# Optimization experiments

Measured on AMD Instinct MI355X. Metric: run time of the kernel, lower is better.

Reference implementation:

```python
import jax, jax.numpy as jnp
import numpy as np

B, M, D = 16384, 32, 16
LAYERS = [64, 64, 64]


def setup_inputs() -> dict:
    key = jax.random.key(0)
    ks = jax.random.split(key, 4)
    inp = {"embeddings": jax.random.normal(ks[0], (B, M, D), dtype=jnp.float32)}
    hk_1 = M
    for i, hk in enumerate(LAYERS):
        # glorot-ish scale for W_i of shape (m, Hk_1, Hk)
        scale = (2.0 / (M * hk_1 + hk)) ** 0.5
        inp[f"W{i}"] = jax.random.normal(ks[i + 1], (M, hk_1, hk), dtype=jnp.float32) * scale
        hk_1 = hk
    return inp


def reference(embeddings, W0, W1, W2):
    # embeddings == x0: (B, m, D); W_i: (m, Hk_1, Hk)
    x0 = embeddings
    xk = x0  # x^{k-1}, starts as x0 with Hk_1 = m
    outs = []
    for W in (W0, W1, W2):
        # Fused form of: (x0[:,:,None,:] * xk[:,None,:,:])[..., None] * W -> sum over m, Hk_1
        # then permute to (B, Hk, D) and apply activation.
        xk = jax.nn.relu(jnp.einsum("bmd,bhd,mhk->bkd", x0, xk, W))  # (B, Hk, D)
        outs.append(jnp.sum(xk, axis=2))  # (B, Hk)
    return jnp.concatenate(outs, axis=1)  # (B, sum(layers_dim))
```

## Files before the change

kernel.cpp:

```cpp
#include <hip/hip_runtime.h>


typedef _Float16 half8 __attribute__((ext_vector_type(8)));
typedef _Float16 half2v __attribute__((ext_vector_type(2)));
typedef float f32x4 __attribute__((ext_vector_type(4)));

#define OUT_STRIDE 192
#define X0R 33
#define X0B (16 * X0R)
#define XKR 72
#define XKB 1152

__global__ void prep_w_all(const float* __restrict__ W0,
                           const float* __restrict__ W1,
                           const float* __restrict__ W2,
                           _Float16* __restrict__ dst) {
  __shared__ float tile[32 * 65];
  const int tid = threadIdx.x;
  const int blk = blockIdx.x;
  const float* src;
  _Float16* d;
  int kb;
  if (blk < 32)      { src = W0 + (size_t)blk * 2048;        d = dst;          kb = blk; }
  else if (blk < 96) { src = W1 + (size_t)(blk - 32) * 2048; d = dst + 65536;  kb = blk - 32; }
  else               { src = W2 + (size_t)(blk - 96) * 2048; d = dst + 196608; kb = blk - 96; }
#pragma unroll
  for (int i = tid; i < 2048; i += 256)
    tile[(i >> 6) * 65 + (i & 63)] = src[i];
  __syncthreads();
  const int lane = tid & 63, t = tid >> 6;
  const int qq = lane >> 4, n = t * 16 + (lane & 15);
  half8 v;
#pragma unroll
  for (int j = 0; j < 8; ++j)
    v[j] = (_Float16)tile[(qq * 8 + j) * 65 + n];
  *(half8*)(d + (size_t)kb * 2048 + tid * 8) = v;
}

template<int NHI, bool LAST>
__device__ __forceinline__ void run_layer(
    const _Float16* __restrict__ Wp, const half8 (&av)[4][NHI],
    const _Float16* x0row0, _Float16* xkw, float* __restrict__ out,
    long gb0, int loff, int lane, int r, int q)
{
  f32x4 acc[4][4];
#pragma unroll
  for (int b = 0; b < 4; ++b)
#pragma unroll
    for (int t = 0; t < 4; ++t) acc[b][t] = (f32x4){0.f, 0.f, 0.f, 0.f};

#pragma unroll 2
  for (int m = 0; m < 32; ++m) {
    half2v xs2[4];
#pragma unroll
    for (int b = 0; b < 4; ++b) {
      _Float16 x = x0row0[b * X0B + m];
      xs2[b] = (half2v){x, x};
    }
#pragma unroll
    for (int hi = 0; hi < NHI; ++hi) {
      const int kb = m * NHI + hi;
      const _Float16* pkb = Wp + (size_t)kb * 2048 + lane * 8;
      half8 Bf[4];
#pragma unroll
      for (int t = 0; t < 4; ++t)
        Bf[t] = *(const half8*)(pkb + t * 512);
#pragma unroll
      for (int b = 0; b < 4; ++b) {
        half8 af;
        half2v* ap = (half2v*)&af;
        const half2v* vp = (const half2v*)&av[b][hi];
#pragma unroll
        for (int j2 = 0; j2 < 4; ++j2) ap[j2] = vp[j2] * xs2[b];
#pragma unroll
        for (int t = 0; t < 4; ++t)
          acc[b][t] = __builtin_amdgcn_mfma_f32_16x16x32_f16(
              af, Bf[t], acc[b][t], 0, 0, 0);
      }
    }
  }

#pragma unroll
  for (int b = 0; b < 4; ++b) {
#pragma unroll
    for (int t = 0; t < 4; ++t) {
      float s = 0.f;
#pragma unroll
      for (int rr = 0; rr < 4; ++rr) {
        float v = acc[b][t][rr];
        v = v > 0.f ? v : 0.f;
        s += v;
        if (!LAST)
          xkw[b * XKB + (q * 4 + rr) * XKR + t * 16 + r] = (_Float16)v;
      }
      s += __shfl_xor(s, 16);
      s += __shfl_xor(s, 32);
      if (q == 0)
        out[(gb0 + b) * OUT_STRIDE + loff + t * 16 + r] = s;
    }
  }
}

__global__ __launch_bounds__(256, 3) void cin_main(
    const float* __restrict__ emb, const _Float16* __restrict__ Wall,
    float* __restrict__ out)
{
  __shared__ __align__(16) _Float16 lds[16 * X0B + 16 * XKB];
  const int lane = threadIdx.x & 63;
  const int wv = threadIdx.x >> 6;
  const int r = lane & 15, q = lane >> 4;
  const long gb0 = (long)blockIdx.x * 16 + wv * 4;

  _Float16* x0w = &lds[wv * 4 * X0B];
  _Float16* xkw = &lds[16 * X0B + wv * 4 * XKB];

#pragma unroll
  for (int bb = 0; bb < 4; ++bb) {
    const float* src = emb + (gb0 + bb) * 512;
    _Float16* dstb = x0w + bb * X0B;
#pragma unroll
    for (int i = 0; i < 2; ++i) {
      int f = i * 256 + lane * 4;
      float4 v = *(const float4*)(src + f);
      int m = f >> 4, d = f & 15;
      dstb[(d + 0) * X0R + m] = (_Float16)v.x;
      dstb[(d + 1) * X0R + m] = (_Float16)v.y;
      dstb[(d + 2) * X0R + m] = (_Float16)v.z;
      dstb[(d + 3) * X0R + m] = (_Float16)v.w;
    }
  }

  const _Float16* x0row0 = x0w + r * X0R;

  half8 av1[4][1];
#pragma unroll
  for (int b = 0; b < 4; ++b)
#pragma unroll
    for (int j = 0; j < 8; ++j)
      av1[b][0][j] = x0row0[b * X0B + q * 8 + j];
  run_layer<1, false>(Wall, av1, x0row0, xkw, out, gb0, 0, lane, r, q);

  half8 av2[4][2];
#pragma unroll
  for (int b = 0; b < 4; ++b)
#pragma unroll
    for (int hi = 0; hi < 2; ++hi)
      av2[b][hi] = *(const half8*)(xkw + b * XKB + r * XKR + hi * 32 + q * 8);
  run_layer<2, false>(Wall + 65536, av2, x0row0, xkw, out, gb0, 64, lane, r, q);

#pragma unroll
  for (int b = 0; b < 4; ++b)
#pragma unroll
    for (int hi = 0; hi < 2; ++hi)
      av2[b][hi] = *(const half8*)(xkw + b * XKB + r * XKR + hi * 32 + q * 8);
  run_layer<2, true>(Wall + 196608, av2, x0row0, xkw, out, gb0, 128, lane, r, q);
}

extern "C" void kernel_launch(void* const* d_in, const int* in_sizes, int n_in,
                              void* d_out, int out_size, void* d_ws, size_t ws_size,
                              hipStream_t stream) {
  const float* emb = (const float*)d_in[0];
  const float* W0  = (const float*)d_in[1];
  const float* W1  = (const float*)d_in[2];
  const float* W2  = (const float*)d_in[3];
  float* out = (float*)d_out;
  _Float16* ws = (_Float16*)d_ws;

  prep_w_all<<<160, 256, 0, stream>>>(W0, W1, W2, ws);

  cin_main<<<1024, 256, 0, stream>>>(emb, ws, out);
}
```

Measured before the change: 209.9 us.

## Double-buffer W fragment loads and stagger m start per wave

Restructures the m-loop into a register double-buffered pipeline that prefetches the next m's weight fragments and x0 scalars while issuing MFMAs on the current ones. Each wave starts at a rotated m offset so waves spread their global weight reads across different addresses. It also uses an inline v_pk_mul_f16 with op_sel to broadcast the x0 scalar, and lowers launch bounds from 3 to 2 waves per SIMD so the extra registers fit. Lower occupancy may expose latency that the prefetching does not cover.

```diff
diff --git a/kernel.cpp b/kernel.cpp
--- a/kernel.cpp
+++ b/kernel.cpp
@@ -10,6 +10,13 @@
 #define X0B (16 * X0R)
 #define XKR 72
 #define XKB 1152
+
+__device__ __forceinline__ half2v pk_mul_bcast(half2v a, unsigned int xs) {
+  half2v r;
+  asm("v_pk_mul_f16 %0, %1, %2 op_sel:[0,0] op_sel_hi:[1,0]"
+      : "=v"(r) : "v"(a), "v"(xs));
+  return r;
+}
 
 __global__ void prep_w_all(const float* __restrict__ W0,
                            const float* __restrict__ W1,
@@ -41,7 +48,7 @@
 __device__ __forceinline__ void run_layer(
     const _Float16* __restrict__ Wp, const half8 (&av)[4][NHI],
     const _Float16* x0row0, _Float16* xkw, float* __restrict__ out,
-    long gb0, int loff, int lane, int r, int q)
+    long gb0, int loff, int lane, int r, int q, int mstart)
 {
   f32x4 acc[4][4];
 #pragma unroll
@@ -49,36 +56,67 @@
 #pragma unroll
     for (int t = 0; t < 4; ++t) acc[b][t] = (f32x4){0.f, 0.f, 0.f, 0.f};
 
-#pragma unroll 2
-  for (int m = 0; m < 32; ++m) {
-    half2v xs2[4];
-#pragma unroll
-    for (int b = 0; b < 4; ++b) {
-      _Float16 x = x0row0[b * X0B + m];
-      xs2[b] = (half2v){x, x};
+  const _Float16* Wl = Wp + lane * 8;
+
+#define LOADB(DST, MM)                                                      \
+  {                                                                         \
+    const _Float16* p_ = Wl + (size_t)(MM) * (NHI * 2048);                  \
+    _Pragma("unroll")                                                       \
+    for (int hi = 0; hi < NHI; ++hi)                                        \
+      _Pragma("unroll")                                                     \
+      for (int t = 0; t < 4; ++t)                                           \
+        DST[hi][t] = *(const half8*)(p_ + hi * 2048 + t * 512);             \
+  }
+
+#define LOADXS(DST, MM)                                                     \
+  {                                                                         \
+    _Pragma("unroll")                                                       \
+    for (int b = 0; b < 4; ++b)                                             \
+      DST[b] = *(const unsigned short*)(x0row0 + b * X0B + (MM));           \
+  }
+
+#define COMPUTE(BB, XX)                                                     \
+  {                                                                         \
+    _Pragma("unroll")                                                       \
+    for (int b = 0; b < 4; ++b) {                                           \
+      _Pragma("unroll")                                                     \
+      for (int hi = 0; hi < NHI; ++hi) {                                    \
+        half8 af;                                                           \
+        half2v* ap = (half2v*)&af;                                          \
+        const half2v* vp = (const half2v*)&av[b][hi];                       \
+        _Pragma("unroll")                                                   \
+        for (int j2 = 0; j2 < 4; ++j2)                                      \
+          ap[j2] = pk_mul_bcast(vp[j2], XX[b]);                             \
+        _Pragma("unroll")                                                   \
+        for (int t = 0; t < 4; ++t)                                         \
+          acc[b][t] = __builtin_amdgcn_mfma_f32_16x16x32_f16(               \
+              af, BB[hi][t], acc[b][t], 0, 0, 0);                           \
+      }                                                                     \
+    }                                                                       \
+  }
+
+  half8 Bc[NHI][4], Bn[NHI][4];
+  unsigned int xc[4], xn[4];
+  const int m0 = mstart;
+
+  LOADB(Bc, m0);
+  LOADXS(xc, m0);
+
+  for (int s = 0; s < 32; s += 2) {
+    const int m1 = (m0 + s + 1) & 31;
+    LOADB(Bn, m1);
+    LOADXS(xn, m1);
+    COMPUTE(Bc, xc);
+    if (s < 30) {
+      const int m2 = (m0 + s + 2) & 31;
+      LOADB(Bc, m2);
+      LOADXS(xc, m2);
     }
-#pragma unroll
-    for (int hi = 0; hi < NHI; ++hi) {
-      const int kb = m * NHI + hi;
-      const _Float16* pkb = Wp + (size_t)kb * 2048 + lane * 8;
-      half8 Bf[4];
-#pragma unroll
-      for (int t = 0; t < 4; ++t)
-        Bf[t] = *(const half8*)(pkb + t * 512);
-#pragma unroll
-      for (int b = 0; b < 4; ++b) {
-        half8 af;
-        half2v* ap = (half2v*)&af;
-        const half2v* vp = (const half2v*)&av[b][hi];
-#pragma unroll
-        for (int j2 = 0; j2 < 4; ++j2) ap[j2] = vp[j2] * xs2[b];
-#pragma unroll
-        for (int t = 0; t < 4; ++t)
-          acc[b][t] = __builtin_amdgcn_mfma_f32_16x16x32_f16(
-              af, Bf[t], acc[b][t], 0, 0, 0);
-      }
-    }
-  }
+    COMPUTE(Bn, xn);
+  }
+#undef LOADB
+#undef LOADXS
+#undef COMPUTE
 
 #pragma unroll
   for (int b = 0; b < 4; ++b) {
@@ -101,7 +139,7 @@
   }
 }
 
-__global__ __launch_bounds__(256, 3) void cin_main(
+__global__ __launch_bounds__(256, 2) void cin_main(
     const float* __restrict__ emb, const _Float16* __restrict__ Wall,
     float* __restrict__ out)
 {
@@ -110,6 +148,8 @@
   const int wv = threadIdx.x >> 6;
   const int r = lane & 15, q = lane >> 4;
   const long gb0 = (long)blockIdx.x * 16 + wv * 4;
+
+  const int mstart = ((blockIdx.x + wv) & 3) * 8;
 
   _Float16* x0w = &lds[wv * 4 * X0B];
   _Float16* xkw = &lds[16 * X0B + wv * 4 * XKB];
@@ -138,7 +178,7 @@
 #pragma unroll
     for (int j = 0; j < 8; ++j)
       av1[b][0][j] = x0row0[b * X0B + q * 8 + j];
-  run_layer<1, false>(Wall, av1, x0row0, xkw, out, gb0, 0, lane, r, q);
+  run_layer<1, false>(Wall, av1, x0row0, xkw, out, gb0, 0, lane, r, q, mstart);
 
   half8 av2[4][2];
 #pragma unroll
@@ -146,14 +186,14 @@
 #pragma unroll
     for (int hi = 0; hi < 2; ++hi)
       av2[b][hi] = *(const half8*)(xkw + b * XKB + r * XKR + hi * 32 + q * 8);
-  run_layer<2, false>(Wall + 65536, av2, x0row0, xkw, out, gb0, 64, lane, r, q);
+  run_layer<2, false>(Wall + 65536, av2, x0row0, xkw, out, gb0, 64, lane, r, q, mstart);
 
 #pragma unroll
   for (int b = 0; b < 4; ++b)
 #pragma unroll
     for (int hi = 0; hi < 2; ++hi)
       av2[b][hi] = *(const half8*)(xkw + b * XKB + r * XKR + hi * 32 + q * 8);
-  run_layer<2, true>(Wall + 196608, av2, x0row0, xkw, out, gb0, 128, lane, r, q);
+  run_layer<2, true>(Wall + 196608, av2, x0row0, xkw, out, gb0, 128, lane, r, q, mstart);
 }
 
 extern "C" void kernel_launch(void* const* d_in, const int* in_sizes, int n_in,
```

New measurement: 224.0 us. 6.7% more time.

## Switch CIN matmuls from 16x16x32 to 32x32x16 MFMA with paired batch rows

Applied to the files above, without the earlier changes.

Replaces the 16x16x32 f16 MFMA tiling with 32x32x16 MFMA. Each A tile now packs two batch elements' 16 D-rows into 32 rows, and the weight prep kernel is re-laid-out to match the 32-wide B fragments. This halves the number of weight fragment loads per MFMA and the MFMA instruction count, aiming for higher matrix-core efficiency. The epilogue remapping and the XK LDS stride change (72 to 64, removing padding) risk more LDS bank conflicts, and the new index mapping adds risk to correctness.

```diff
diff --git a/kernel.cpp b/kernel.cpp
--- a/kernel.cpp
+++ b/kernel.cpp
@@ -3,13 +3,13 @@
 
 typedef _Float16 half8 __attribute__((ext_vector_type(8)));
 typedef _Float16 half2v __attribute__((ext_vector_type(2)));
-typedef float f32x4 __attribute__((ext_vector_type(4)));
+typedef float f32x16 __attribute__((ext_vector_type(16)));
 
 #define OUT_STRIDE 192
 #define X0R 33
 #define X0B (16 * X0R)
-#define XKR 72
-#define XKB 1152
+#define XKR 64
+#define XKB 1024
 
 __global__ void prep_w_all(const float* __restrict__ W0,
                            const float* __restrict__ W1,
@@ -20,83 +20,92 @@
   const int blk = blockIdx.x;
   const float* src;
   _Float16* d;
-  int kb;
-  if (blk < 32)      { src = W0 + (size_t)blk * 2048;        d = dst;          kb = blk; }
-  else if (blk < 96) { src = W1 + (size_t)(blk - 32) * 2048; d = dst + 65536;  kb = blk - 32; }
-  else               { src = W2 + (size_t)(blk - 96) * 2048; d = dst + 196608; kb = blk - 96; }
+  int bl;
+  if (blk < 32)      { src = W0; d = dst;          bl = blk; }
+  else if (blk < 96) { src = W1; d = dst + 65536;  bl = blk - 32; }
+  else               { src = W2; d = dst + 196608; bl = blk - 96; }
+  src += (size_t)bl * 2048;
+  d   += (size_t)bl * 2048;
 #pragma unroll
   for (int i = tid; i < 2048; i += 256)
     tile[(i >> 6) * 65 + (i & 63)] = src[i];
   __syncthreads();
-  const int lane = tid & 63, t = tid >> 6;
-  const int qq = lane >> 4, n = t * 16 + (lane & 15);
+  const int sub  = tid >> 7;
+  const int t    = (tid >> 6) & 1;
+  const int lane = tid & 63;
+  const int q2 = lane >> 5, l31 = lane & 31;
   half8 v;
 #pragma unroll
   for (int j = 0; j < 8; ++j)
-    v[j] = (_Float16)tile[(qq * 8 + j) * 65 + n];
-  *(half8*)(d + (size_t)kb * 2048 + tid * 8) = v;
+    v[j] = (_Float16)tile[(sub * 16 + q2 * 8 + j) * 65 + t * 32 + l31];
+  *(half8*)(d + ((sub * 2 + t) * 64 + lane) * 8) = v;
 }
 
-template<int NHI, bool LAST>
+template<int NHB, bool LAST>
 __device__ __forceinline__ void run_layer(
-    const _Float16* __restrict__ Wp, const half8 (&av)[4][NHI],
-    const _Float16* x0row0, _Float16* xkw, float* __restrict__ out,
-    long gb0, int loff, int lane, int r, int q)
+    const _Float16* __restrict__ Wp, const half8 (&av)[2][NHB],
+    const _Float16* const (&xsb)[2], _Float16* xkw, float* __restrict__ out,
+    long gb0, int loff, int lane)
 {
-  f32x4 acc[4][4];
+  const int q2 = lane >> 5, l31 = lane & 31;
+
+  f32x16 acc[2][2];
 #pragma unroll
-  for (int b = 0; b < 4; ++b)
+  for (int bp = 0; bp < 2; ++bp)
 #pragma unroll
-    for (int t = 0; t < 4; ++t) acc[b][t] = (f32x4){0.f, 0.f, 0.f, 0.f};
+    for (int t = 0; t < 2; ++t)
+#pragma unroll
+      for (int g = 0; g < 16; ++g) acc[bp][t][g] = 0.f;
+
+  const _Float16* Wl = Wp + lane * 8;
 
 #pragma unroll 2
   for (int m = 0; m < 32; ++m) {
-    half2v xs2[4];
+    half2v xs2[2];
 #pragma unroll
-    for (int b = 0; b < 4; ++b) {
-      _Float16 x = x0row0[b * X0B + m];
-      xs2[b] = (half2v){x, x};
+    for (int bp = 0; bp < 2; ++bp) {
+      _Float16 x = xsb[bp][m];
+      xs2[bp] = (half2v){x, x};
     }
 #pragma unroll
-    for (int hi = 0; hi < NHI; ++hi) {
-      const int kb = m * NHI + hi;
-      const _Float16* pkb = Wp + (size_t)kb * 2048 + lane * 8;
-      half8 Bf[4];
+    for (int hb = 0; hb < NHB; ++hb) {
+      const int kb = m * NHB + hb;
+      const _Float16* p = Wl + (size_t)kb * 1024;
+      half8 B0 = *(const half8*)(p);
+      half8 B1 = *(const half8*)(p + 512);
 #pragma unroll
-      for (int t = 0; t < 4; ++t)
-        Bf[t] = *(const half8*)(pkb + t * 512);
-#pragma unroll
-      for (int b = 0; b < 4; ++b) {
+      for (int bp = 0; bp < 2; ++bp) {
         half8 af;
         half2v* ap = (half2v*)&af;
-        const half2v* vp = (const half2v*)&av[b][hi];
+        const half2v* vp = (const half2v*)&av[bp][hb];
 #pragma unroll
-        for (int j2 = 0; j2 < 4; ++j2) ap[j2] = vp[j2] * xs2[b];
-#pragma unroll
-        for (int t = 0; t < 4; ++t)
-          acc[b][t] = __builtin_amdgcn_mfma_f32_16x16x32_f16(
-              af, Bf[t], acc[b][t], 0, 0, 0);
+        for (int j2 = 0; j2 < 4; ++j2) ap[j2] = vp[j2] * xs2[bp];
+        acc[bp][0] = __builtin_amdgcn_mfma_f32_32x32x16_f16(af, B0, acc[bp][0], 0, 0, 0);
+        acc[bp][1] = __builtin_amdgcn_mfma_f32_32x32x16_f16(af, B1, acc[bp][1], 0, 0, 0);
       }
     }
   }
 
 #pragma unroll
-  for (int b = 0; b < 4; ++b) {
+  for (int bp = 0; bp < 2; ++bp) {
 #pragma unroll
-    for (int t = 0; t < 4; ++t) {
-      float s = 0.f;
+    for (int t = 0; t < 2; ++t) {
+      float s[2] = {0.f, 0.f};
 #pragma unroll
-      for (int rr = 0; rr < 4; ++rr) {
-        float v = acc[b][t][rr];
+      for (int g = 0; g < 16; ++g) {
+        float v = acc[bp][t][g];
         v = v > 0.f ? v : 0.f;
-        s += v;
+        const int half = g >> 3;
+        const int g7 = g & 7;
+        const int d = (g7 & 3) + 8 * (g7 >> 2) + 4 * q2;
+        s[half] += v;
         if (!LAST)
-          xkw[b * XKB + (q * 4 + rr) * XKR + t * 16 + r] = (_Float16)v;
+          xkw[(bp * 2 + half) * XKB + d * XKR + t * 32 + l31] = (_Float16)v;
       }
-      s += __shfl_xor(s, 16);
-      s += __shfl_xor(s, 32);
-      if (q == 0)
-        out[(gb0 + b) * OUT_STRIDE + loff + t * 16 + r] = s;
+      s[0] += __shfl_xor(s[0], 32);
+      s[1] += __shfl_xor(s[1], 32);
+      const float sv = q2 ? s[1] : s[0];
+      out[(gb0 + bp * 2 + q2) * OUT_STRIDE + loff + t * 32 + l31] = sv;
     }
   }
 }
@@ -108,7 +117,9 @@
   __shared__ __align__(16) _Float16 lds[16 * X0B + 16 * XKB];
   const int lane = threadIdx.x & 63;
   const int wv = threadIdx.x >> 6;
-  const int r = lane & 15, q = lane >> 4;
+  const int r16 = lane & 15;
+  const int q2 = lane >> 5;
+  const int bhalf = (lane >> 4) & 1;
   const long gb0 = (long)blockIdx.x * 16 + wv * 4;
 
   _Float16* x0w = &lds[wv * 4 * X0B];
@@ -130,30 +141,37 @@
     }
   }
 
-  const _Float16* x0row0 = x0w + r * X0R;
+  const _Float16* xsb[2] = {
+    x0w + (0 + bhalf) * X0B + r16 * X0R,
+    x0w + (2 + bhalf) * X0B + r16 * X0R,
+  };
 
-  half8 av1[4][1];
+  half8 av1[2][2];
 #pragma unroll
-  for (int b = 0; b < 4; ++b)
+  for (int bp = 0; bp < 2; ++bp)
 #pragma unroll
-    for (int j = 0; j < 8; ++j)
-      av1[b][0][j] = x0row0[b * X0B + q * 8 + j];
-  run_layer<1, false>(Wall, av1, x0row0, xkw, out, gb0, 0, lane, r, q);
+    for (int hb = 0; hb < 2; ++hb)
+#pragma unroll
+      for (int j = 0; j < 8; ++j)
+        av1[bp][hb][j] = xsb[bp][hb * 16 + q2 * 8 + j];
+  run_layer<2, false>(Wall, av1, xsb, xkw, out, gb0, 0, lane);
 
-  half8 av2[4][2];
+  half8 av2[2][4];
 #pragma unroll
-  for (int b = 0; b < 4; ++b)
+  for (int bp = 0; bp < 2; ++bp)
 #pragma unroll
-    for (int hi = 0; hi < 2; ++hi)
-      av2[b][hi] = *(const half8*)(xkw + b * XKB + r * XKR + hi * 32 + q * 8);
-  run_layer<2, false>(Wall + 65536, av2, x0row0, xkw, out, gb0, 64, lane, r, q);
+    for (int hb = 0; hb < 4; ++hb)
+      av2[bp][hb] = *(const half8*)(xkw + (bp * 2 + bhalf) * XKB +
+                                    r16 * XKR + hb * 16 + q2 * 8);
+  run_layer<4, false>(Wall + 65536, av2, xsb, xkw, out, gb0, 64, lane);
 
 #pragma unroll
-  for (int b = 0; b < 4; ++b)
+  for (int bp = 0; bp < 2; ++bp)
 #pragma unroll
-    for (int hi = 0; hi < 2; ++hi)
-      av2[b][hi] = *(const half8*)(xkw + b * XKB + r * XKR + hi * 32 + q * 8);
-  run_layer<2, true>(Wall + 196608, av2, x0row0, xkw, out, gb0, 128, lane, r, q);
+    for (int hb = 0; hb < 4; ++hb)
+      av2[bp][hb] = *(const half8*)(xkw + (bp * 2 + bhalf) * XKB +
+                                    r16 * XKR + hb * 16 + q2 * 8);
+  run_layer<4, true>(Wall + 196608, av2, xsb, xkw, out, gb0, 128, lane);
 }
 
 extern "C" void kernel_launch(void* const* d_in, const int* in_sizes, int n_in,
```

New measurement: 232.7 us. 1.11x slower.
